# Performance work log

Measured on AMD Instinct MI355X. Metric: run time of the kernel, lower is better.

The kernel has to match this reference:

```python
import jax, jax.numpy as jnp
import numpy as np

N = 100000   # nodes
D = 128      # embedding_dim
E = 1600000  # edges
L = 3        # num_layers


def setup_inputs() -> dict:
    key = jax.random.key(0)
    ks = jax.random.split(key, 10)
    s = 1.0 / np.sqrt(D)
    def w(k, shape):
        return jax.random.uniform(k, shape, jnp.float32, -s, s)
    return {
        "x": jax.random.normal(ks[0], (N, D), jnp.float32),
        "edge_index": jax.random.randint(ks[1], (2, E), 0, N, jnp.int32),
        "Wp": w(ks[2], (L - 1, D, D)),   # project Linear weight (per layer)
        "bp": w(ks[3], (L - 1, D)),      # project Linear bias
        "Wl": w(ks[4], (L - 1, D, D)),   # lin_l (aggregated neighbors)
        "bl": w(ks[5], (L - 1, D)),
        "Wr": w(ks[6], (L - 1, D, D)),   # lin_r (root, no bias)
        "Wl_out": w(ks[7], (D, D)),
        "bl_out": w(ks[8], (D,)),
        "Wr_out": w(ks[9], (D, D)),
    }


def _sage(x, src, dst, inv_deg, Wl, bl, Wr, Wp=None, bp=None, normalize=False):
    # PyG SAGEConv: project applies to messages only; root term uses original x.
    h = jax.nn.relu(x @ Wp.T + bp) if Wp is not None else x
    agg = jax.ops.segment_sum(h[src], dst, num_segments=N) * inv_deg  # mean aggr
    out = agg @ Wl.T + bl + x @ Wr.T
    if normalize:
        out = out / jnp.maximum(
            jnp.linalg.norm(out, axis=-1, keepdims=True), 1e-12)
    return out


def reference(x, edge_index, Wp, bp, Wl, bl, Wr, Wl_out, bl_out, Wr_out):
    src, dst = edge_index[0], edge_index[1]
    deg = jax.ops.segment_sum(jnp.ones((src.shape[0],), x.dtype), dst,
                              num_segments=N)
    inv_deg = (1.0 / jnp.maximum(deg, 1.0))[:, None]  # isolated nodes -> 0 agg
    for i in range(L - 1):
        x = jax.nn.relu(
            _sage(x, src, dst, inv_deg, Wl[i], bl[i], Wr[i], Wp[i], bp[i],
                  normalize=True))
    return _sage(x, src, dst, inv_deg, Wl_out, bl_out, Wr_out)
```

## Files before the change

### kernel.cpp

```cpp
#include <hip/hip_runtime.h>
#include <math.h>

#define D 128

typedef short s8v __attribute__((ext_vector_type(8)));
typedef float f32x4 __attribute__((ext_vector_type(4)));
typedef float f32x2 __attribute__((ext_vector_type(2)));
typedef unsigned short u16x8 __attribute__((ext_vector_type(8)));

__device__ __forceinline__ unsigned short f2bf(float f) {
  union { float f; unsigned u; } c; c.f = f;
  unsigned u = c.u;
  unsigned r = (u + 0x7fffu + ((u >> 16) & 1u)) >> 16;
  return (unsigned short)r;
}
__device__ __forceinline__ float bf2f(unsigned short b) {
  union { unsigned u; float f; } c; c.u = ((unsigned)b) << 16;
  return c.f;
}

__global__ __launch_bounds__(256) void k_cvt_w(const float* __restrict__ Wp,
                                               const float* __restrict__ Wl,
                                               const float* __restrict__ Wr,
                                               const float* __restrict__ Wlo,
                                               const float* __restrict__ Wro,
                                               unsigned short* __restrict__ Wb,
                                               int* __restrict__ bucketCnt) {
  int i = blockIdx.x * 256 + threadIdx.x;
  const float* s;
  int off;
  if (i < 8192)       { s = Wp;  off = 0; }
  else if (i < 16384) { s = Wl;  off = 8192; }
  else if (i < 24576) { s = Wr;  off = 16384; }
  else if (i < 28672) { s = Wlo; off = 24576; }
  else                { s = Wro; off = 28672; }
  float4 a = ((const float4*)s)[i - off];
  ushort4 o;
  o.x = f2bf(a.x); o.y = f2bf(a.y); o.z = f2bf(a.z); o.w = f2bf(a.w);
  ((ushort4*)Wb)[i] = o;
  if (i < 512) bucketCnt[i] = 0;
}

__global__ __launch_bounds__(256) void k_bucket_count(const int* __restrict__ dst,
                                                      int* __restrict__ bucketCnt, int E_) {
  __shared__ int hist[512];
  int t = threadIdx.x;
  hist[t] = 0; hist[t + 256] = 0;
  __syncthreads();
  int base = blockIdx.x * 4096;
#pragma unroll
  for (int i = 0; i < 16; i++) {
    int e = base + i * 256 + t;
    if (e < E_) atomicAdd(&hist[dst[e] >> 8], 1);
  }
  __syncthreads();
  int c = hist[t];       if (c) atomicAdd(&bucketCnt[t], c);
  c = hist[t + 256];     if (c) atomicAdd(&bucketCnt[t + 256], c);
}

__global__ __launch_bounds__(512) void k_bucket_scan(const int* __restrict__ cnt,
                                                     int* __restrict__ base,
                                                     int* __restrict__ cursor,
                                                     int* __restrict__ row_start,
                                                     int n, int E_) {
  __shared__ int bs[512];
  int t = threadIdx.x;
  int orig = cnt[t];
  bs[t] = orig;
  __syncthreads();
  for (int off = 1; off < 512; off <<= 1) {
    int x = (t >= off) ? bs[t - off] : 0;
    __syncthreads();
    bs[t] += x;
    __syncthreads();
  }
  int ex = bs[t] - orig;
  base[t] = ex;
  cursor[t] = ex;
  if (t == 511) base[512] = bs[511];
  if (t == 0) row_start[n] = E_;
}

__global__ __launch_bounds__(1024) void k_partA(const int* __restrict__ src,
                                                const int* __restrict__ dst,
                                                int* __restrict__ cursor,
                                                int2* __restrict__ pairs, int E_) {
  __shared__ int hist[512];
  __shared__ int gbase[512];
  int t = threadIdx.x;
  int base = blockIdx.x * 16384;
  if (t < 512) hist[t] = 0;
  __syncthreads();
  int s_[16], d_[16];
#pragma unroll
  for (int i = 0; i < 16; i++) {
    int e = base + i * 1024 + t;
    if (e < E_) {
      s_[i] = src[e];
      d_[i] = dst[e];
      atomicAdd(&hist[d_[i] >> 8], 1);
    } else {
      d_[i] = -1;
    }
  }
  __syncthreads();
  if (t < 512) {
    int c = hist[t];
    gbase[t] = c ? atomicAdd(&cursor[t], c) : 0;
    hist[t] = 0;
  }
  __syncthreads();
#pragma unroll
  for (int i = 0; i < 16; i++) {
    if (d_[i] >= 0) {
      int k = d_[i] >> 8;
      int r = atomicAdd(&hist[k], 1);
      pairs[gbase[k] + r] = make_int2(s_[i], d_[i]);
    }
  }
}

__global__ __launch_bounds__(256) void k_partB(const int2* __restrict__ pairs,
                                               const int* __restrict__ bucketBase,
                                               int* __restrict__ row_start,
                                               int* __restrict__ csr, int n) {
  __shared__ int cnt[256];
  __shared__ int scn[256];
  int k = blockIdx.x, t = threadIdx.x;
  int node0 = k << 8;
  int pbeg = bucketBase[k], pend = bucketBase[k + 1];
  cnt[t] = 0;
  __syncthreads();
  for (int p = pbeg + t; p < pend; p += 256) atomicAdd(&cnt[pairs[p].y & 255], 1);
  __syncthreads();
  int c = cnt[t];
  scn[t] = c;
  __syncthreads();
  for (int off = 1; off < 256; off <<= 1) {
    int x = (t >= off) ? scn[t - off] : 0;
    __syncthreads();
    scn[t] += x;
    __syncthreads();
  }
  int ex = scn[t] - c;
  int node = node0 + t;
  if (node < n) row_start[node] = pbeg + ex;
  __syncthreads();
  cnt[t] = pbeg + ex;
  __syncthreads();
  for (int p = pbeg + t; p < pend; p += 256) {
    int2 pr = pairs[p];
    int slot = atomicAdd(&cnt[pr.y & 255], 1);
    csr[slot] = pr.x;
  }
}

__global__ __launch_bounds__(256) void k_aggregate(const unsigned short* __restrict__ h,
                                                   unsigned short* __restrict__ agg,
                                                   const int* __restrict__ row_start,
                                                   const int* __restrict__ csr, int n) {
  int w = (blockIdx.x * 256 + threadIdx.x) >> 6;
  int lane = threadIdx.x & 63;
  if (w >= n) return;
  int rs0 = row_start[w];
  int dc = row_start[w + 1] - rs0;
  int grp = lane >> 4, li = lane & 15;
  const char* base = (const char*)h + li * 16;
  const int* ce = csr + rs0;

  f32x2 acc[4];
#pragma unroll
  for (int q = 0; q < 4; q++) acc[q] = (f32x2){0.f, 0.f};

#define ACC4(v)                                                        \
  {                                                                    \
    unsigned dw[4] = {(v).x, (v).y, (v).z, (v).w};                     \
    _Pragma("unroll") for (int q = 0; q < 4; q++) {                    \
      f32x2 tt;                                                        \
      tt.x = __uint_as_float(dw[q] << 16);                             \
      tt.y = __uint_as_float(dw[q] & 0xffff0000u);                     \
      acc[q] += tt;                                                    \
    }                                                                  \
  }

  int e = grp;
  bool more = (e + 12 < dc);
  int s0 = 0, s1 = 0, s2 = 0, s3 = 0;
  if (more) { s0 = ce[e]; s1 = ce[e + 4]; s2 = ce[e + 8]; s3 = ce[e + 12]; }
  while (more) {
    uint4 v0 = *(const uint4*)(base + (size_t)s0 * 256);
    uint4 v1 = *(const uint4*)(base + (size_t)s1 * 256);
    uint4 v2 = *(const uint4*)(base + (size_t)s2 * 256);
    uint4 v3 = *(const uint4*)(base + (size_t)s3 * 256);
    e += 16;
    more = (e + 12 < dc);
    if (more) { s0 = ce[e]; s1 = ce[e + 4]; s2 = ce[e + 8]; s3 = ce[e + 12]; }
    ACC4(v0); ACC4(v1); ACC4(v2); ACC4(v3);
  }
  if (e < dc) {
    uint4 v = *(const uint4*)(base + (size_t)ce[e] * 256);
    ACC4(v);
  }
  if (e + 4 < dc) {
    uint4 v = *(const uint4*)(base + (size_t)ce[e + 4] * 256);
    ACC4(v);
  }
  if (e + 8 < dc) {
    uint4 v = *(const uint4*)(base + (size_t)ce[e + 8] * 256);
    ACC4(v);
  }
#undef ACC4

#pragma unroll
  for (int q = 0; q < 4; q++) {
    acc[q].x += __shfl_xor(acc[q].x, 16);
    acc[q].y += __shfl_xor(acc[q].y, 16);
    acc[q].x += __shfl_xor(acc[q].x, 32);
    acc[q].y += __shfl_xor(acc[q].y, 32);
  }
  if (grp == 0) {
    float iv = 1.0f / (float)(dc > 0 ? dc : 1);
    u16x8 o;
#pragma unroll
    for (int q = 0; q < 4; q++) {
      o[2 * q] = f2bf(acc[q].x * iv);
      o[2 * q + 1] = f2bf(acc[q].y * iv);
    }
    *(u16x8*)(agg + (size_t)w * D + li * 8) = o;
  }
}

__device__ __forceinline__ int swz_chunk(int r, int c) { return (r << 4) + (c ^ (r & 7)); }

template <int CVT>
__global__ __launch_bounds__(512, 4) void k_gemm_proj(const void* __restrict__ Av,
                                                      const unsigned short* __restrict__ W,
                                                      const float* __restrict__ bias,
                                                      unsigned short* __restrict__ out,
                                                      unsigned short* __restrict__ xb_out,
                                                      int n) {
  __shared__ __align__(16) unsigned short Wlds[128 * 128];
  int t = threadIdx.x;
#pragma unroll
  for (int i = 0; i < 4; ++i) {
    int idx = t + i * 512;
    int r = idx >> 4, k = idx & 15;
    int c = k ^ (r & 7);
    *(u16x8*)&Wlds[idx * 8] = *(const u16x8*)(W + r * 128 + c * 8);
  }
  __syncthreads();

  int wv = t >> 6, l = t & 63, lg = l >> 4, ln = l & 15;
  int rb = blockIdx.x * 128 + wv * 16;
  int arow = rb + ln;
  if (arow >= n) arow = n - 1;

  s8v a[4];
  if (CVT) {
    const float* Af = (const float*)Av + (size_t)arow * D + lg * 8;
#pragma unroll
    for (int ks = 0; ks < 4; ++ks) {
      float4 f0 = *(const float4*)(Af + ks * 32);
      float4 f1 = *(const float4*)(Af + ks * 32 + 4);
      s8v av;
      av[0] = (short)f2bf(f0.x); av[1] = (short)f2bf(f0.y);
      av[2] = (short)f2bf(f0.z); av[3] = (short)f2bf(f0.w);
      av[4] = (short)f2bf(f1.x); av[5] = (short)f2bf(f1.y);
      av[6] = (short)f2bf(f1.z); av[7] = (short)f2bf(f1.w);
      a[ks] = av;
      if (xb_out) *(s8v*)(xb_out + (size_t)arow * D + lg * 8 + ks * 32) = av;
    }
  } else {
    const s8v* Ap = (const s8v*)((const unsigned short*)Av + (size_t)arow * D + lg * 8);
#pragma unroll
    for (int ks = 0; ks < 4; ++ks) a[ks] = Ap[ks * 4];
  }

  f32x4 acc[8];
#pragma unroll
  for (int f = 0; f < 8; ++f) acc[f] = (f32x4){0.f, 0.f, 0.f, 0.f};
#pragma unroll
  for (int ks = 0; ks < 4; ++ks) {
#pragma unroll
    for (int f = 0; f < 8; ++f) {
      s8v b = *(const s8v*)&Wlds[swz_chunk(f * 16 + ln, ks * 4 + lg) * 8];
      acc[f] = __builtin_amdgcn_mfma_f32_16x16x32_bf16(a[ks], b, acc[f], 0, 0, 0);
    }
  }

#pragma unroll
  for (int r = 0; r < 4; ++r) {
    int gr = rb + 4 * lg + r;
    if (gr < n) {
#pragma unroll
      for (int f = 0; f < 8; ++f) {
        int c = f * 16 + ln;
        float v = acc[f][r] + bias[c];
        v = fmaxf(v, 0.f);
        out[(size_t)gr * D + c] = f2bf(v);
      }
    }
  }
}

template <int MODE>
__global__ __launch_bounds__(512, 4) void k_gemm_dual(const unsigned short* __restrict__ A1,
                                                      const unsigned short* __restrict__ W1,
                                                      const float* __restrict__ bias,
                                                      const unsigned short* __restrict__ A2,
                                                      const unsigned short* __restrict__ W2,
                                                      void* __restrict__ outv, int n) {
  __shared__ __align__(16) unsigned short Wlds[2 * 128 * 128];
  int t = threadIdx.x;
#pragma unroll
  for (int i = 0; i < 8; ++i) {
    int idx = t + i * 512;
    int mat = idx >> 11;
    int rem = idx & 2047;
    int r = rem >> 4, k = rem & 15;
    int c = k ^ (r & 7);
    const unsigned short* src = (mat ? W2 : W1) + r * 128 + c * 8;
    *(u16x8*)&Wlds[idx * 8] = *(const u16x8*)src;
  }
  __syncthreads();

  int wv = t >> 6, l = t & 63, lg = l >> 4, ln = l & 15;
  int rb = blockIdx.x * 128 + wv * 16;
  int arow = rb + ln;
  if (arow >= n) arow = n - 1;
  const s8v* A1p = (const s8v*)(A1 + (size_t)arow * D + lg * 8);
  const s8v* A2p = (const s8v*)(A2 + (size_t)arow * D + lg * 8);
  s8v a1[4], a2[4];
#pragma unroll
  for (int ks = 0; ks < 4; ++ks) { a1[ks] = A1p[ks * 4]; a2[ks] = A2p[ks * 4]; }

  f32x4 acc[8];
#pragma unroll
  for (int f = 0; f < 8; ++f) acc[f] = (f32x4){0.f, 0.f, 0.f, 0.f};

#pragma unroll
  for (int ks = 0; ks < 4; ++ks) {
#pragma unroll
    for (int f = 0; f < 8; ++f) {
      int ch = swz_chunk(f * 16 + ln, ks * 4 + lg) * 8;
      s8v b1 = *(const s8v*)&Wlds[ch];
      s8v b2 = *(const s8v*)&Wlds[16384 + ch];
      acc[f] = __builtin_amdgcn_mfma_f32_16x16x32_bf16(a1[ks], b1, acc[f], 0, 0, 0);
      acc[f] = __builtin_amdgcn_mfma_f32_16x16x32_bf16(a2[ks], b2, acc[f], 0, 0, 0);
    }
  }

#pragma unroll
  for (int r = 0; r < 4; ++r) {
    int gr = rb + 4 * lg + r;
    float v[8];
#pragma unroll
    for (int f = 0; f < 8; ++f) v[f] = acc[f][r] + bias[f * 16 + ln];
    if (MODE == 0) {
      float ss = 0.f;
#pragma unroll
      for (int f = 0; f < 8; ++f) ss += v[f] * v[f];
      ss += __shfl_xor(ss, 1);
      ss += __shfl_xor(ss, 2);
      ss += __shfl_xor(ss, 4);
      ss += __shfl_xor(ss, 8);
      float sc = 1.0f / fmaxf(sqrtf(ss), 1e-12f);
      if (gr < n) {
        unsigned short* out = (unsigned short*)outv;
#pragma unroll
        for (int f = 0; f < 8; ++f) {
          float o = fmaxf(v[f] * sc, 0.f);
          out[(size_t)gr * D + f * 16 + ln] = f2bf(o);
        }
      }
    } else {
      if (gr < n) {
        float* out = (float*)outv;
#pragma unroll
        for (int f = 0; f < 8; ++f) out[(size_t)gr * D + f * 16 + ln] = v[f];
      }
    }
  }
}

extern "C" void kernel_launch(void* const* d_in, const int* in_sizes, int n_in,
                              void* d_out, int out_size, void* d_ws, size_t ws_size,
                              hipStream_t stream) {
  const float* x   = (const float*)d_in[0];
  const int*   ei  = (const int*)d_in[1];
  const float* Wp  = (const float*)d_in[2];
  const float* bp  = (const float*)d_in[3];
  const float* Wl  = (const float*)d_in[4];
  const float* bl  = (const float*)d_in[5];
  const float* Wr  = (const float*)d_in[6];
  const float* Wlo = (const float*)d_in[7];
  const float* blo = (const float*)d_in[8];
  const float* Wro = (const float*)d_in[9];

  const int N = in_sizes[0] / D;
  const int E = in_sizes[1] / 2;
  const int* srcIdx = ei;
  const int* dstIdx = ei + E;

  const size_t ND = (size_t)N * D;

  unsigned short* xb   = (unsigned short*)d_ws;
  unsigned short* h    = xb + ND;
  unsigned short* aggB = h + ND;
  unsigned short* x2   = aggB + ND;
  unsigned short* Wb   = x2 + ND;
  int* row_start  = (int*)(Wb + 8 * 16384);
  int* bucketCnt  = row_start + N + 1;
  int* bucketBase = bucketCnt + 512;
  int* cursor     = bucketBase + 513;
  int* csr        = cursor + 512;

  int2* pairs = (int2*)aggB;

  unsigned short* Wpb0 = Wb;
  unsigned short* Wpb1 = Wb + 16384;
  unsigned short* Wlb0 = Wb + 2 * 16384;
  unsigned short* Wlb1 = Wb + 3 * 16384;
  unsigned short* Wrb0 = Wb + 4 * 16384;
  unsigned short* Wrb1 = Wb + 5 * 16384;
  unsigned short* Wlob = Wb + 6 * 16384;
  unsigned short* Wrob = Wb + 7 * 16384;

  unsigned short* x1 = (unsigned short*)d_out;

  int gG = (N + 127) / 128;
  int gW = (N + 3) / 4;
  int KB = (N + 255) / 256;
  int gBC = (E + 4095) / 4096;
  int gA  = (E + 16383) / 16384;

  k_cvt_w<<<128, 256, 0, stream>>>(Wp, Wl, Wr, Wlo, Wro, Wb, bucketCnt);

  k_bucket_count<<<gBC, 256, 0, stream>>>(dstIdx, bucketCnt, E);
  k_bucket_scan<<<1, 512, 0, stream>>>(bucketCnt, bucketBase, cursor, row_start, N, E);
  k_partA<<<gA, 1024, 0, stream>>>(srcIdx, dstIdx, cursor, pairs, E);
  k_partB<<<KB, 256, 0, stream>>>(pairs, bucketBase, row_start, csr, N);

  k_gemm_proj<1><<<gG, 512, 0, stream>>>(x, Wpb0, bp, h, xb, N);
  k_aggregate<<<gW, 256, 0, stream>>>(h, aggB, row_start, csr, N);
  k_gemm_dual<0><<<gG, 512, 0, stream>>>(aggB, Wlb0, bl, xb, Wrb0, (void*)x1, N);

  k_gemm_proj<0><<<gG, 512, 0, stream>>>(x1, Wpb1, bp + D, h, nullptr, N);
  k_aggregate<<<gW, 256, 0, stream>>>(h, aggB, row_start, csr, N);
  k_gemm_dual<0><<<gG, 512, 0, stream>>>(aggB, Wlb1, bl + D, x1, Wrb1, (void*)x2, N);

  k_aggregate<<<gW, 256, 0, stream>>>(x2, aggB, row_start, csr, N);
  k_gemm_dual<1><<<gG, 512, 0, stream>>>(aggB, Wlob, blo, x2, Wrob, d_out, N);
}
```

Before: 334.5 us.

## Fuse weight conversion with bucket count, pack edge pairs, use direct LDS loads

Result: no change. 340.5 us (+1.8%).

```diff
diff --git a/kernel.cpp b/kernel.cpp
--- a/kernel.cpp
+++ b/kernel.cpp
@@ -14,48 +14,48 @@
   unsigned r = (u + 0x7fffu + ((u >> 16) & 1u)) >> 16;
   return (unsigned short)r;
 }
-__device__ __forceinline__ float bf2f(unsigned short b) {
-  union { unsigned u; float f; } c; c.u = ((unsigned)b) << 16;
-  return c.f;
-}
-
-__global__ __launch_bounds__(256) void k_cvt_w(const float* __restrict__ Wp,
-                                               const float* __restrict__ Wl,
-                                               const float* __restrict__ Wr,
-                                               const float* __restrict__ Wlo,
-                                               const float* __restrict__ Wro,
-                                               unsigned short* __restrict__ Wb,
-                                               int* __restrict__ bucketCnt) {
-  int i = blockIdx.x * 256 + threadIdx.x;
-  const float* s;
-  int off;
-  if (i < 8192)       { s = Wp;  off = 0; }
-  else if (i < 16384) { s = Wl;  off = 8192; }
-  else if (i < 24576) { s = Wr;  off = 16384; }
-  else if (i < 28672) { s = Wlo; off = 24576; }
-  else                { s = Wro; off = 28672; }
-  float4 a = ((const float4*)s)[i - off];
-  ushort4 o;
-  o.x = f2bf(a.x); o.y = f2bf(a.y); o.z = f2bf(a.z); o.w = f2bf(a.w);
-  ((ushort4*)Wb)[i] = o;
-  if (i < 512) bucketCnt[i] = 0;
-}
-
-__global__ __launch_bounds__(256) void k_bucket_count(const int* __restrict__ dst,
-                                                      int* __restrict__ bucketCnt, int E_) {
-  __shared__ int hist[512];
+
+__device__ __forceinline__ void gload_lds16(const void* g, void* l) {
+  __builtin_amdgcn_global_load_lds((const __attribute__((address_space(1))) void*)g,
+                                   (__attribute__((address_space(3))) void*)l, 16, 0, 0);
+}
+
+__global__ __launch_bounds__(256) void k_prep(const float* __restrict__ Wp,
+                                              const float* __restrict__ Wl,
+                                              const float* __restrict__ Wr,
+                                              const float* __restrict__ Wlo,
+                                              const float* __restrict__ Wro,
+                                              unsigned short* __restrict__ Wb,
+                                              const int* __restrict__ dst,
+                                              int* __restrict__ bucketCnt, int E_) {
   int t = threadIdx.x;
-  hist[t] = 0; hist[t + 256] = 0;
-  __syncthreads();
-  int base = blockIdx.x * 4096;
-#pragma unroll
-  for (int i = 0; i < 16; i++) {
-    int e = base + i * 256 + t;
-    if (e < E_) atomicAdd(&hist[dst[e] >> 8], 1);
-  }
-  __syncthreads();
-  int c = hist[t];       if (c) atomicAdd(&bucketCnt[t], c);
-  c = hist[t + 256];     if (c) atomicAdd(&bucketCnt[t + 256], c);
+  if (blockIdx.x < 128) {
+    int i = blockIdx.x * 256 + t;
+    const float* s;
+    int off;
+    if (i < 8192)       { s = Wp;  off = 0; }
+    else if (i < 16384) { s = Wl;  off = 8192; }
+    else if (i < 24576) { s = Wr;  off = 16384; }
+    else if (i < 28672) { s = Wlo; off = 24576; }
+    else                { s = Wro; off = 28672; }
+    float4 a = ((const float4*)s)[i - off];
+    ushort4 o;
+    o.x = f2bf(a.x); o.y = f2bf(a.y); o.z = f2bf(a.z); o.w = f2bf(a.w);
+    ((ushort4*)Wb)[i] = o;
+  } else {
+    __shared__ int hist[512];
+    hist[t] = 0; hist[t + 256] = 0;
+    __syncthreads();
+    int base = (blockIdx.x - 128) * 4096;
+#pragma unroll
+    for (int i = 0; i < 16; i++) {
+      int e = base + i * 256 + t;
+      if (e < E_) atomicAdd(&hist[dst[e] >> 8], 1);
+    }
+    __syncthreads();
+    int c = hist[t];       if (c) atomicAdd(&bucketCnt[t], c);
+    c = hist[t + 256];     if (c) atomicAdd(&bucketCnt[t + 256], c);
+  }
 }
 
 __global__ __launch_bounds__(512) void k_bucket_scan(const int* __restrict__ cnt,
@@ -84,23 +84,25 @@
 __global__ __launch_bounds__(1024) void k_partA(const int* __restrict__ src,
                                                 const int* __restrict__ dst,
                                                 int* __restrict__ cursor,
-                                                int2* __restrict__ pairs, int E_) {
+                                                unsigned* __restrict__ pairs, int E_) {
   __shared__ int hist[512];
   __shared__ int gbase[512];
   int t = threadIdx.x;
   int base = blockIdx.x * 16384;
   if (t < 512) hist[t] = 0;
   __syncthreads();
-  int s_[16], d_[16];
+  unsigned p_[16];
+  int k_[16];
 #pragma unroll
   for (int i = 0; i < 16; i++) {
     int e = base + i * 1024 + t;
     if (e < E_) {
-      s_[i] = src[e];
-      d_[i] = dst[e];
-      atomicAdd(&hist[d_[i] >> 8], 1);
+      int s = src[e], d = dst[e];
+      p_[i] = ((unsigned)s << 8) | (unsigned)(d & 255);
+      k_[i] = d >> 8;
+      atomicAdd(&hist[k_[i]], 1);
     } else {
-      d_[i] = -1;
+      k_[i] = -1;
     }
   }
   __syncthreads();
@@ -112,15 +114,14 @@
   __syncthreads();
 #pragma unroll
   for (int i = 0; i < 16; i++) {
-    if (d_[i] >= 0) {
-      int k = d_[i] >> 8;
-      int r = atomicAdd(&hist[k], 1);
-      pairs[gbase[k] + r] = make_int2(s_[i], d_[i]);
-    }
-  }
-}
-
-__global__ __launch_bounds__(256) void k_partB(const int2* __restrict__ pairs,
+    if (k_[i] >= 0) {
+      int r = atomicAdd(&hist[k_[i]], 1);
+      pairs[gbase[k_[i]] + r] = p_[i];
+    }
+  }
+}
+
+__global__ __launch_bounds__(256) void k_partB(const unsigned* __restrict__ pairs,
                                                const int* __restrict__ bucketBase,
                                                int* __restrict__ row_start,
                                                int* __restrict__ csr, int n) {
@@ -131,7 +132,7 @@
   int pbeg = bucketBase[k], pend = bucketBase[k + 1];
   cnt[t] = 0;
   __syncthreads();
-  for (int p = pbeg + t; p < pend; p += 256) atomicAdd(&cnt[pairs[p].y & 255], 1);
+  for (int p = pbeg + t; p < pend; p += 256) atomicAdd(&cnt[pairs[p] & 255], 1);
   __syncthreads();
   int c = cnt[t];
   scn[t] = c;
@@ -149,9 +150,9 @@
   cnt[t] = pbeg + ex;
   __syncthreads();
   for (int p = pbeg + t; p < pend; p += 256) {
-    int2 pr = pairs[p];
-    int slot = atomicAdd(&cnt[pr.y & 255], 1);
-    csr[slot] = pr.x;
+    unsigned pr = pairs[p];
+    int slot = atomicAdd(&cnt[pr & 255], 1);
+    csr[slot] = (int)(pr >> 8);
   }
 }
 
@@ -178,7 +179,7 @@
     _Pragma("unroll") for (int q = 0; q < 4; q++) {                    \
       f32x2 tt;                                                        \
       tt.x = __uint_as_float(dw[q] << 16);                             \
-      tt.y = __uint_as_float(dw[q] & 0xffff0000u);                     \
+      tt.y = __uint_as_float(dw[q]);                                   \
       acc[q] += tt;                                                    \
     }                                                                  \
   }
@@ -241,15 +242,6 @@
                                                       int n) {
   __shared__ __align__(16) unsigned short Wlds[128 * 128];
   int t = threadIdx.x;
-#pragma unroll
-  for (int i = 0; i < 4; ++i) {
-    int idx = t + i * 512;
-    int r = idx >> 4, k = idx & 15;
-    int c = k ^ (r & 7);
-    *(u16x8*)&Wlds[idx * 8] = *(const u16x8*)(W + r * 128 + c * 8);
-  }
-  __syncthreads();
-
   int wv = t >> 6, l = t & 63, lg = l >> 4, ln = l & 15;
   int rb = blockIdx.x * 128 + wv * 16;
   int arow = rb + ln;
@@ -276,6 +268,15 @@
     for (int ks = 0; ks < 4; ++ks) a[ks] = Ap[ks * 4];
   }
 
+#pragma unroll
+  for (int i = 0; i < 4; ++i) {
+    int idx = t + i * 512;
+    int r = idx >> 4, k = idx & 15;
+    int c = k ^ (r & 7);
+    gload_lds16(W + r * 128 + c * 8, &Wlds[idx * 8]);
+  }
+  __syncthreads();
+
   f32x4 acc[8];
 #pragma unroll
   for (int f = 0; f < 8; ++f) acc[f] = (f32x4){0.f, 0.f, 0.f, 0.f};
@@ -312,6 +313,16 @@
                                                       void* __restrict__ outv, int n) {
   __shared__ __align__(16) unsigned short Wlds[2 * 128 * 128];
   int t = threadIdx.x;
+  int wv = t >> 6, l = t & 63, lg = l >> 4, ln = l & 15;
+  int rb = blockIdx.x * 128 + wv * 16;
+  int arow = rb + ln;
+  if (arow >= n) arow = n - 1;
+  const s8v* A1p = (const s8v*)(A1 + (size_t)arow * D + lg * 8);
+  const s8v* A2p = (const s8v*)(A2 + (size_t)arow * D + lg * 8);
+  s8v a1[4], a2[4];
+#pragma unroll
+  for (int ks = 0; ks < 4; ++ks) { a1[ks] = A1p[ks * 4]; a2[ks] = A2p[ks * 4]; }
+
 #pragma unroll
   for (int i = 0; i < 8; ++i) {
     int idx = t + i * 512;
@@ -320,19 +331,9 @@
     int r = rem >> 4, k = rem & 15;
     int c = k ^ (r & 7);
     const unsigned short* src = (mat ? W2 : W1) + r * 128 + c * 8;
-    *(u16x8*)&Wlds[idx * 8] = *(const u16x8*)src;
-  }
-  __syncthreads();
-
-  int wv = t >> 6, l = t & 63, lg = l >> 4, ln = l & 15;
-  int rb = blockIdx.x * 128 + wv * 16;
-  int arow = rb + ln;
-  if (arow >= n) arow = n - 1;
-  const s8v* A1p = (const s8v*)(A1 + (size_t)arow * D + lg * 8);
-  const s8v* A2p = (const s8v*)(A2 + (size_t)arow * D + lg * 8);
-  s8v a1[4], a2[4];
-#pragma unroll
-  for (int ks = 0; ks < 4; ++ks) { a1[ks] = A1p[ks * 4]; a2[ks] = A2p[ks * 4]; }
+    gload_lds16(src, &Wlds[idx * 8]);
+  }
+  __syncthreads();
 
   f32x4 acc[8];
 #pragma unroll
@@ -415,7 +416,7 @@
   int* cursor     = bucketBase + 513;
   int* csr        = cursor + 512;
 
-  int2* pairs = (int2*)aggB;
+  unsigned* pairs = (unsigned*)aggB;
 
   unsigned short* Wpb0 = Wb;
   unsigned short* Wpb1 = Wb + 16384;
@@ -434,9 +435,9 @@
   int gBC = (E + 4095) / 4096;
   int gA  = (E + 16383) / 16384;
 
-  k_cvt_w<<<128, 256, 0, stream>>>(Wp, Wl, Wr, Wlo, Wro, Wb, bucketCnt);
-
-  k_bucket_count<<<gBC, 256, 0, stream>>>(dstIdx, bucketCnt, E);
+  hipMemsetAsync(bucketCnt, 0, 512 * sizeof(int), stream);
+  k_prep<<<128 + gBC, 256, 0, stream>>>(Wp, Wl, Wr, Wlo, Wro, Wb, dstIdx, bucketCnt, E);
+
   k_bucket_scan<<<1, 512, 0, stream>>>(bucketCnt, bucketBase, cursor, row_start, N, E);
   k_partA<<<gA, 1024, 0, stream>>>(srcIdx, dstIdx, cursor, pairs, E);
   k_partB<<<KB, 256, 0, stream>>>(pairs, bucketBase, row_start, csr, N);
```
